# Kernel optimization log

Hardware: AMD Instinct MI355X
Metric: run time of the kernel (lower is better)

The kernel has to match this reference:

```python
import jax, jax.numpy as jnp
import numpy as np

B, N, C, NUM_HEADS = 4, 2048, 768, 12
HID = 4 * C
EPS = 1e-5


def _ln(x, g, b):
    m = x.mean(-1, keepdims=True)
    v = ((x - m) ** 2).mean(-1, keepdims=True)
    return (x - m) / jnp.sqrt(v + EPS) * g + b


def _attend(q, k, v, scale):
    # q,k,v: (B, H, N, D)
    scores = jnp.einsum('bhnd,bhmd->bhnm', q, k) * scale
    a = jax.nn.softmax(scores, axis=-1)
    return jnp.einsum('bhnm,bhmd->bhnd', a, v)


def _split_heads(t):
    b, n, c = t.shape
    return t.reshape(b, n, NUM_HEADS, c // NUM_HEADS).transpose(0, 2, 1, 3)


def _merge_heads(t):
    b, h, n, d = t.shape
    return t.transpose(0, 2, 1, 3).reshape(b, n, h * d)


def setup_inputs() -> dict:
    key = jax.random.key(0)
    ks = jax.random.split(key, 16)
    s = 0.02
    inp = {
        'x': jax.random.normal(ks[0], (B, N, C), jnp.float32),
        'y': jax.random.normal(ks[1], (B, N, C), jnp.float32),
        'xpos': jax.random.randint(ks[2], (B, N, 2), 0, 64, jnp.int32),
        'ypos': jax.random.randint(ks[3], (B, N, 2), 0, 64, jnp.int32),
        'g1': jnp.ones((C,)), 'be1': jnp.zeros((C,)),
        'g2': jnp.ones((C,)), 'be2': jnp.zeros((C,)),
        'g3': jnp.ones((C,)), 'be3': jnp.zeros((C,)),
        'gy': jnp.ones((C,)), 'bey': jnp.zeros((C,)),
        'Wqkv': jax.random.normal(ks[4], (C, 3 * C), jnp.float32) * s,
        'Wo_sa': jax.random.normal(ks[5], (C, C), jnp.float32) * s,
        'bo_sa': jnp.zeros((C,)),
        'Wq': jax.random.normal(ks[6], (C, C), jnp.float32) * s,
        'Wk': jax.random.normal(ks[7], (C, C), jnp.float32) * s,
        'Wv': jax.random.normal(ks[8], (C, C), jnp.float32) * s,
        'Wo_ca': jax.random.normal(ks[9], (C, C), jnp.float32) * s,
        'bo_ca': jnp.zeros((C,)),
        'W1': jax.random.normal(ks[10], (C, HID), jnp.float32) * s,
        'b1': jnp.zeros((HID,)),
        'W2': jax.random.normal(ks[11], (HID, C), jnp.float32) * s,
        'b2': jnp.zeros((C,)),
        'h': 32, 'w': 64,
    }
    return inp


def reference(x, y, xpos, ypos, g1, be1, g2, be2, g3, be3, gy, bey,
              Wqkv, Wo_sa, bo_sa, Wq, Wk, Wv, Wo_ca, bo_ca,
              W1, b1, W2, b2, h, w):
    scale = (C // NUM_HEADS) ** -0.5
    # --- self attention (rope=None, dropout=0, drop_path=0) ---
    xn = _ln(x, g1, be1)
    qkv = (xn @ Wqkv).reshape(x.shape[0], x.shape[1], 3, C)
    q, k, v = (_split_heads(qkv[:, :, i]) for i in range(3))
    o = _merge_heads(_attend(q, k, v, scale)) @ Wo_sa + bo_sa
    x = x + o
    # --- cross attention ---
    yn = _ln(y, gy, bey)
    xn2 = _ln(x, g2, be2)
    qc = _split_heads(xn2 @ Wq)
    kc = _split_heads(yn @ Wk)
    vc = _split_heads(yn @ Wv)
    oc = _merge_heads(_attend(qc, kc, vc, scale)) @ Wo_ca + bo_ca
    x = x + oc
    # --- MLP (exact GELU as torch nn.GELU default) ---
    xn3 = _ln(x, g3, be3)
    x = x + (jax.nn.gelu(xn3 @ W1 + b1, approximate=False) @ W2 + b2)
    return x
```

## Files before the change

### kernel.cpp

```cpp
#include <hip/hip_runtime.h>
#include <math.h>

typedef unsigned short u16;
typedef __attribute__((ext_vector_type(4))) float f32x4;
typedef __attribute__((ext_vector_type(8))) __bf16 bf16x8;
typedef __attribute__((ext_vector_type(8))) short s16x8;

#define AS1 __attribute__((address_space(1)))
#define AS3 __attribute__((address_space(3)))

__device__ __forceinline__ u16 cvt(float f) {
  __bf16 h = (__bf16)f;
  return *(u16*)&h;
}

__device__ __forceinline__ unsigned cvtpk(float lo, float hi) {
  unsigned r;
  asm("v_cvt_pk_bf16_f32 %0, %1, %2" : "=v"(r) : "v"(lo), "v"(hi));
  return r;
}

__device__ __forceinline__ float fexp2(float x) {
  float r;
  asm volatile("v_exp_f32 %0, %1" : "=v"(r) : "v"(x));
  return r;
}

__device__ __forceinline__ void load_lds16(const void* g, void* l) {
  __builtin_amdgcn_global_load_lds((AS1 void*)g, (AS3 void*)l, 16, 0, 0);
}

__device__ __forceinline__ f32x4 mfma16(bf16x8 a, bf16x8 b, f32x4 c) {
  return __builtin_amdgcn_mfma_f32_16x16x32_bf16(a, b, c, 0, 0, 0);
}

struct WT8 {
  const float* src[8];
  u16* dst[8];
  int K[8];
  int N[8];
  int cnt[8];
};

__global__ void wtrans_all(WT8 a) {
  __shared__ float t[32][33];
  int rem = blockIdx.x, i = 0;
  while (rem >= a.cnt[i]) { rem -= a.cnt[i]; ++i; }
  const int nb = a.N[i] >> 5;
  const int n0 = (rem % nb) * 32, k0 = (rem / nb) * 32;
  const float* W = a.src[i];
  u16* WT = a.dst[i];
  const int K = a.K[i], N = a.N[i];
  for (int r = threadIdx.y; r < 32; r += 8)
    t[r][threadIdx.x] = W[(size_t)(k0 + r) * N + n0 + threadIdx.x];
  __syncthreads();
  for (int r = threadIdx.y; r < 32; r += 8)
    WT[(size_t)(n0 + r) * K + k0 + threadIdx.x] = cvt(t[threadIdx.x][r]);
}

__global__ __launch_bounds__(256)
void ln_bf16(const float* __restrict__ in, const float* __restrict__ g,
             const float* __restrict__ be, u16* __restrict__ out) {
  const int row = blockIdx.x, tid = threadIdx.x;
  const float* x = in + (size_t)row * 768;
  float v0 = x[tid], v1 = x[tid + 256], v2 = x[tid + 512];
  float s = v0 + v1 + v2;
  for (int m = 1; m < 64; m <<= 1) s += __shfl_xor(s, m);
  __shared__ float red[8];
  const int w = tid >> 6, lane = tid & 63;
  if (lane == 0) red[w] = s;
  __syncthreads();
  s = red[0] + red[1] + red[2] + red[3];
  const float mean = s * (1.f / 768.f);
  const float d0 = v0 - mean, d1 = v1 - mean, d2 = v2 - mean;
  float q = d0 * d0 + d1 * d1 + d2 * d2;
  for (int m = 1; m < 64; m <<= 1) q += __shfl_xor(q, m);
  if (lane == 0) red[4 + w] = q;
  __syncthreads();
  q = red[4] + red[5] + red[6] + red[7];
  const float rstd = rsqrtf(q * (1.f / 768.f) + 1e-5f);
  u16* o = out + (size_t)row * 768;
  o[tid]       = cvt(d0 * rstd * g[tid]       + be[tid]);
  o[tid + 256] = cvt(d1 * rstd * g[tid + 256] + be[tid + 256]);
  o[tid + 512] = cvt(d2 * rstd * g[tid + 512] + be[tid + 512]);
}

template <int EPI, int BM>
__global__ __launch_bounds__(256, BM == 128 ? 2 : 3)
void gemm_bt(const u16* __restrict__ A, const u16* __restrict__ BT,
             const float* __restrict__ bias, const float* resid,
             void* outp, int M, int N, int K, int ldc) {
  constexpr int NI = (BM == 128) ? 4 : 2;
  constexpr int BK = (BM == 128) ? 32 : 64;
  __shared__ u16 As[BM * BK];
  __shared__ u16 Bs[128 * BK];
  const int tid = threadIdx.x;
  const int lane = tid & 63, w = tid >> 6;
  const int lr = lane & 15, g = lane >> 4;

  int bx = blockIdx.x, by = blockIdx.y;
  if (BM == 64) {
    const int nwg = gridDim.x * gridDim.y;
    if ((nwg & 7) == 0) {
      const int d = by * gridDim.x + bx;
      const int l = (d & 7) * (nwg >> 3) + (d >> 3);
      bx = l % gridDim.x;
      by = l / gridDim.x;
    }
  }
  const int row0 = by * BM, col0 = bx * 128;
  const int wm = (BM == 128) ? (w >> 1) * 64 : 0;
  const int wn = (BM == 128) ? (w & 1) * 64 : w * 32;

  f32x4 acc[4][NI] = {};

  if (BM == 128) {
    const int srow = lane >> 2, scol = (lane & 3) * 8;
    const int lk = g * 8;
    for (int k0 = 0; k0 < K; k0 += 32) {
#pragma unroll
      for (int i = 0; i < 2; ++i) {
        const int chunk = w * 2 + i;
        load_lds16(A + (size_t)(row0 + chunk * 16 + srow) * K + k0 + scol, &As[chunk * 512]);
        load_lds16(BT + (size_t)(col0 + chunk * 16 + srow) * K + k0 + scol, &Bs[chunk * 512]);
      }
      __syncthreads();
      bf16x8 af[4], bf[NI];
#pragma unroll
      for (int mi = 0; mi < 4; ++mi) af[mi] = *(const bf16x8*)&As[(wm + mi * 16 + lr) * 32 + lk];
#pragma unroll
      for (int ni = 0; ni < NI; ++ni) bf[ni] = *(const bf16x8*)&Bs[(wn + ni * 16 + lr) * 32 + lk];
#pragma unroll
      for (int mi = 0; mi < 4; ++mi)
#pragma unroll
        for (int ni = 0; ni < NI; ++ni)
          acc[mi][ni] = mfma16(af[mi], bf[ni], acc[mi][ni]);
      __syncthreads();
    }
  } else {
    for (int k0 = 0; k0 < K; k0 += 64) {
#pragma unroll
      for (int i = 0; i < 2; ++i) {
        const int ch = i * 256 + tid;
        const int r = ch >> 3, c = ch & 7, cs = c ^ (r & 7);
        load_lds16(A + (size_t)(row0 + r) * K + k0 + cs * 8, &As[ch * 8]);
      }
#pragma unroll
      for (int i = 0; i < 4; ++i) {
        const int ch = i * 256 + tid;
        const int r = ch >> 3, c = ch & 7, cs = c ^ (r & 7);
        load_lds16(BT + (size_t)(col0 + r) * K + k0 + cs * 8, &Bs[ch * 8]);
      }
      __syncthreads();
#pragma unroll
      for (int kk = 0; kk < 2; ++kk) {
        bf16x8 af[4], bf[NI];
#pragma unroll
        for (int mi = 0; mi < 4; ++mi) {
          const int r = mi * 16 + lr;
          af[mi] = *(const bf16x8*)&As[r * 64 + (((kk * 4 + g) ^ (r & 7)) * 8)];
        }
#pragma unroll
        for (int ni = 0; ni < NI; ++ni) {
          const int r = wn + ni * 16 + lr;
          bf[ni] = *(const bf16x8*)&Bs[r * 64 + (((kk * 4 + g) ^ (r & 7)) * 8)];
        }
#pragma unroll
        for (int mi = 0; mi < 4; ++mi)
#pragma unroll
          for (int ni = 0; ni < NI; ++ni)
            acc[mi][ni] = mfma16(af[mi], bf[ni], acc[mi][ni]);
      }
      __syncthreads();
    }
  }

  const int rbase = g * 4;
#pragma unroll
  for (int mi = 0; mi < 4; ++mi) {
#pragma unroll
    for (int ni = 0; ni < NI; ++ni) {
#pragma unroll
      for (int rr = 0; rr < 4; ++rr) {
        const int r = row0 + wm + mi * 16 + rbase + rr;
        const int c = col0 + wn + ni * 16 + lr;
        float v = acc[mi][ni][rr];
        if (EPI == 0) {
          ((u16*)outp)[(size_t)r * ldc + c] = cvt(v);
        } else if (EPI == 1) {
          ((float*)outp)[(size_t)r * ldc + c] = v + bias[c] + resid[(size_t)r * ldc + c];
        } else {
          v += bias[c];
          v = 0.5f * v * (1.f + erff(v * 0.70710678118654752f));
          ((u16*)outp)[(size_t)r * ldc + c] = cvt(v);
        }
      }
    }
  }
}

__global__ __launch_bounds__(256, 3)
void flash_attn(const u16* __restrict__ qk, const u16* __restrict__ vt, u16* __restrict__ out) {
  __shared__ u16 Ks[2][64 * 64];
  __shared__ u16 Vs[2][64 * 64];
  __shared__ u16 P[128 * 72];
  const int tid = threadIdx.x, lane = tid & 63, w = tid >> 6;
  const int b = blockIdx.z, h = blockIdx.y, qb = blockIdx.x;
  const u16* qp = qk + (size_t)b * 2048 * 1536 + h * 64;
  const u16* kp = qp + 768;
  const u16* vtp = vt + (size_t)(h * 64) * 8192 + b * 2048;
  const int lr = lane & 15, g = lane >> 4, lk = g * 8;
  const int qrow = qb * 128 + w * 32;

  bf16x8 qf[2][2];
#pragma unroll
  for (int gq = 0; gq < 2; ++gq) {
#pragma unroll
    for (int t = 0; t < 2; ++t) {
      s16x8 qr = *(const s16x8*)&qp[(size_t)(qrow + gq * 16 + lr) * 1536 + t * 32 + lk];
      bf16x8 f;
#pragma unroll
      for (int j = 0; j < 8; ++j) {
        unsigned u = (unsigned)(u16)qr[j] << 16;
        f[j] = (__bf16)(__uint_as_float(u) * 0.18033688f);
      }
      qf[gq][t] = f;
    }
  }

  bf16x8 onesf;
#pragma unroll
  for (int j = 0; j < 8; ++j) onesf[j] = (__bf16)1.0f;

  f32x4 o[2][4] = {};
  f32x4 o4[2] = {};
  float rowm[2] = {-1e30f, -1e30f};

#define STAGE(bi, kv)                                                          \
  do {                                                                         \
    _Pragma("unroll") for (int i_ = 0; i_ < 2; ++i_) {                         \
      const int ch = i_ * 256 + tid;                                           \
      const int r_ = ch >> 3, c_ = ch & 7, cs_ = c_ ^ (r_ & 7);                \
      load_lds16(kp + (size_t)((kv) + r_) * 1536 + cs_ * 8, &Ks[bi][ch * 8]);  \
      load_lds16(vtp + (size_t)r_ * 8192 + (kv) + cs_ * 8, &Vs[bi][ch * 8]);   \
    }                                                                          \
  } while (0)

  STAGE(0, 0);
  __syncthreads();
  int cur = 0;

  for (int kv0 = 0; kv0 < 2048; kv0 += 64) {
    if (kv0 + 64 < 2048) STAGE(cur ^ 1, kv0 + 64);

    f32x4 s[2][4] = {};
#pragma unroll
    for (int t = 0; t < 2; ++t) {
#pragma unroll
      for (int ni = 0; ni < 4; ++ni) {
        const int r = ni * 16 + lr;
        bf16x8 kf = *(const bf16x8*)&Ks[cur][r * 64 + ((4 * t + g) ^ (lr & 7)) * 8];
        s[0][ni] = mfma16(kf, qf[0][t], s[0][ni]);
        s[1][ni] = mfma16(kf, qf[1][t], s[1][ni]);
      }
    }

    float lm[2];
#pragma unroll
    for (int gq = 0; gq < 2; ++gq) {
      float m0 = fmaxf(fmaxf(s[gq][0][0], s[gq][0][1]), fmaxf(s[gq][0][2], s[gq][0][3]));
      float m1 = fmaxf(fmaxf(s[gq][1][0], s[gq][1][1]), fmaxf(s[gq][1][2], s[gq][1][3]));
      float m2 = fmaxf(fmaxf(s[gq][2][0], s[gq][2][1]), fmaxf(s[gq][2][2], s[gq][2][3]));
      float m3 = fmaxf(fmaxf(s[gq][3][0], s[gq][3][1]), fmaxf(s[gq][3][2], s[gq][3][3]));
      lm[gq] = fmaxf(fmaxf(m0, m1), fmaxf(m2, m3));
    }
    const int ok = (lm[0] <= rowm[0] + 8.f) & (lm[1] <= rowm[1] + 8.f);
    if (!__all(ok)) {
#pragma unroll
      for (int gq = 0; gq < 2; ++gq) {
        float v = lm[gq];
        v = fmaxf(v, __shfl_xor(v, 16));
        v = fmaxf(v, __shfl_xor(v, 32));
        const float mn = fmaxf(rowm[gq], v);
        const float alpha = fexp2(rowm[gq] - mn);
        rowm[gq] = mn;
#pragma unroll
        for (int di = 0; di < 4; ++di) o[gq][di] *= alpha;
        o4[gq] *= alpha;
      }
    }

    unsigned* Pw = (unsigned*)P;
#pragma unroll
    for (int gq = 0; gq < 2; ++gq) {
      const int qrl = w * 32 + gq * 16 + lr;
#pragma unroll
      for (int ni = 0; ni < 4; ++ni) {
#pragma unroll
        for (int r = 0; r < 2; ++r) {
          const float p0 = fexp2(s[gq][ni][2 * r] - rowm[gq]);
          const float p1 = fexp2(s[gq][ni][2 * r + 1] - rowm[gq]);
          Pw[(qrl * 72 + ni * 16 + 4 * g + 2 * r) >> 1] = cvtpk(p0, p1);
        }
      }
    }

#pragma unroll
    for (int t = 0; t < 2; ++t) {
      bf16x8 pb0 = *(const bf16x8*)&P[(w * 32 + lr) * 72 + t * 32 + g * 8];
      bf16x8 pb1 = *(const bf16x8*)&P[(w * 32 + 16 + lr) * 72 + t * 32 + g * 8];
#pragma unroll
      for (int di = 0; di < 4; ++di) {
        bf16x8 va = *(const bf16x8*)&Vs[cur][(di * 16 + lr) * 64 + ((4 * t + g) ^ (lr & 7)) * 8];
        o[0][di] = mfma16(va, pb0, o[0][di]);
        o[1][di] = mfma16(va, pb1, o[1][di]);
      }
      o4[0] = mfma16(onesf, pb0, o4[0]);
      o4[1] = mfma16(onesf, pb1, o4[1]);
    }

    __syncthreads();
    cur ^= 1;
  }
#undef STAGE

#pragma unroll
  for (int gq = 0; gq < 2; ++gq) {
    const float inv = 1.0f / o4[gq][0];
    const size_t n = (size_t)b * 2048 + qrow + gq * 16 + lr;
#pragma unroll
    for (int di = 0; di < 4; ++di) {
      uint2 uv;
      uv.x = cvtpk(o[gq][di][0] * inv, o[gq][di][1] * inv);
      uv.y = cvtpk(o[gq][di][2] * inv, o[gq][di][3] * inv);
      *(uint2*)&out[n * 768 + h * 64 + di * 16 + 4 * g] = uv;
    }
  }
}

extern "C" void kernel_launch(void* const* d_in, const int* in_sizes, int n_in,
                              void* d_out, int out_size, void* d_ws, size_t ws_size,
                              hipStream_t stream) {
  const float* x     = (const float*)d_in[0];
  const float* y     = (const float*)d_in[1];
  const float* g1    = (const float*)d_in[4];
  const float* be1   = (const float*)d_in[5];
  const float* g2    = (const float*)d_in[6];
  const float* be2   = (const float*)d_in[7];
  const float* g3    = (const float*)d_in[8];
  const float* be3   = (const float*)d_in[9];
  const float* gy    = (const float*)d_in[10];
  const float* bey   = (const float*)d_in[11];
  const float* Wqkv  = (const float*)d_in[12];
  const float* Wo_sa = (const float*)d_in[13];
  const float* bo_sa = (const float*)d_in[14];
  const float* Wq    = (const float*)d_in[15];
  const float* Wk    = (const float*)d_in[16];
  const float* Wv    = (const float*)d_in[17];
  const float* Wo_ca = (const float*)d_in[18];
  const float* bo_ca = (const float*)d_in[19];
  const float* W1    = (const float*)d_in[20];
  const float* b1    = (const float*)d_in[21];
  const float* W2    = (const float*)d_in[22];
  const float* b2    = (const float*)d_in[23];

  u16* WqkvT = (u16*)d_ws;
  u16* WoSaT = WqkvT + (size_t)2304 * 768;
  u16* WqT   = WoSaT + (size_t)768 * 768;
  u16* WkT   = WqT   + (size_t)768 * 768;
  u16* WvT   = WkT   + (size_t)768 * 768;
  u16* WoCaT = WvT   + (size_t)768 * 768;
  u16* W1T   = WoCaT + (size_t)768 * 768;
  u16* W2T   = W1T   + (size_t)3072 * 768;
  u16* R1    = W2T   + (size_t)768 * 3072;
  u16* VT    = R1    + (size_t)8192 * 1536;
  u16* R2    = R1    + (size_t)8192 * 3072;
  u16* R3    = R2    + (size_t)8192 * 768;
  float* xo  = (float*)d_out;

  WT8 wa;
  {
    const float* s8[8] = {Wqkv, Wo_sa, Wq, Wk, Wv, Wo_ca, W1, W2};
    u16* d8[8] = {WqkvT, WoSaT, WqT, WkT, WvT, WoCaT, W1T, W2T};
    const int K8[8] = {768, 768, 768, 768, 768, 768, 768, 3072};
    const int N8[8] = {2304, 768, 768, 768, 768, 768, 3072, 768};
    for (int i = 0; i < 8; ++i) {
      wa.src[i] = s8[i]; wa.dst[i] = d8[i];
      wa.K[i] = K8[i]; wa.N[i] = N8[i];
      wa.cnt[i] = (N8[i] / 32) * (K8[i] / 32);
    }
  }
  wtrans_all<<<9216, dim3(32, 8), 0, stream>>>(wa);

  ln_bf16<<<8192, 256, 0, stream>>>(x, g1, be1, R2);
  gemm_bt<0, 128><<<dim3(12, 64), 256, 0, stream>>>(R2, WqkvT, nullptr, nullptr, R1, 8192, 1536, 768, 1536);
  gemm_bt<0, 64><<<dim3(64, 12), 256, 0, stream>>>(WqkvT + (size_t)1536 * 768, R2, nullptr, nullptr, VT, 768, 8192, 768, 8192);
  flash_attn<<<dim3(16, 12, 4), 256, 0, stream>>>(R1, VT, R2);
  gemm_bt<1, 64><<<dim3(6, 128), 256, 0, stream>>>(R2, WoSaT, bo_sa, x, xo, 8192, 768, 768, 768);

  ln_bf16<<<8192, 256, 0, stream>>>(y, gy, bey, R3);
  ln_bf16<<<8192, 256, 0, stream>>>(xo, g2, be2, R2);
  gemm_bt<0, 64><<<dim3(6, 128), 256, 0, stream>>>(R2, WqT, nullptr, nullptr, R1, 8192, 768, 768, 1536);
  gemm_bt<0, 64><<<dim3(6, 128), 256, 0, stream>>>(R3, WkT, nullptr, nullptr, R1 + 768, 8192, 768, 768, 1536);
  gemm_bt<0, 64><<<dim3(64, 12), 256, 0, stream>>>(WvT, R3, nullptr, nullptr, VT, 768, 8192, 768, 8192);
  flash_attn<<<dim3(16, 12, 4), 256, 0, stream>>>(R1, VT, R3);
  gemm_bt<1, 64><<<dim3(6, 128), 256, 0, stream>>>(R3, WoCaT, bo_ca, xo, xo, 8192, 768, 768, 768);

  ln_bf16<<<8192, 256, 0, stream>>>(xo, g3, be3, R2);
  gemm_bt<2, 128><<<dim3(24, 64), 256, 0, stream>>>(R2, W1T, b1, nullptr, R1, 8192, 3072, 768, 3072);
  gemm_bt<1, 64><<<dim3(6, 128), 256, 0, stream>>>(R1, W2T, b2, xo, xo, 8192, 768, 3072, 768);
}
```

Before: 467.9 us.

## Unify GEMM on BK=64 swizzled path and tweak attention softmax stores

The BM=128 GEMM variant now uses the BK=64 XOR-swizzled LDS path instead of BK=32 unswizzled tiles, with launch bounds raised to 3 and the grid remapping applied to all tile sizes. In the attention kernel, P values are written as one 64-bit store per fragment instead of two 32-bit stores, and the max reduction is reshaped. The PV MFMA section is also wrapped in s_setprio to favor matrix issue. The larger LDS tile and higher occupancy target may raise register pressure for the 128-row GEMM.

```diff
diff --git a/kernel.cpp b/kernel.cpp
--- a/kernel.cpp
+++ b/kernel.cpp
@@ -86,20 +86,19 @@
 }
 
 template <int EPI, int BM>
-__global__ __launch_bounds__(256, BM == 128 ? 2 : 3)
+__global__ __launch_bounds__(256, 3)
 void gemm_bt(const u16* __restrict__ A, const u16* __restrict__ BT,
              const float* __restrict__ bias, const float* resid,
              void* outp, int M, int N, int K, int ldc) {
   constexpr int NI = (BM == 128) ? 4 : 2;
-  constexpr int BK = (BM == 128) ? 32 : 64;
-  __shared__ u16 As[BM * BK];
-  __shared__ u16 Bs[128 * BK];
+  __shared__ u16 As[BM * 64];
+  __shared__ u16 Bs[128 * 64];
   const int tid = threadIdx.x;
   const int lane = tid & 63, w = tid >> 6;
   const int lr = lane & 15, g = lane >> 4;
 
   int bx = blockIdx.x, by = blockIdx.y;
-  if (BM == 64) {
+  {
     const int nwg = gridDim.x * gridDim.y;
     if ((nwg & 7) == 0) {
       const int d = by * gridDim.x + bx;
@@ -114,65 +113,40 @@
 
   f32x4 acc[4][NI] = {};
 
-  if (BM == 128) {
-    const int srow = lane >> 2, scol = (lane & 3) * 8;
-    const int lk = g * 8;
-    for (int k0 = 0; k0 < K; k0 += 32) {
-#pragma unroll
-      for (int i = 0; i < 2; ++i) {
-        const int chunk = w * 2 + i;
-        load_lds16(A + (size_t)(row0 + chunk * 16 + srow) * K + k0 + scol, &As[chunk * 512]);
-        load_lds16(BT + (size_t)(col0 + chunk * 16 + srow) * K + k0 + scol, &Bs[chunk * 512]);
-      }
-      __syncthreads();
+  for (int k0 = 0; k0 < K; k0 += 64) {
+#pragma unroll
+    for (int i = 0; i < BM / 32; ++i) {
+      const int ch = i * 256 + tid;
+      const int r = ch >> 3, c = ch & 7, cs = c ^ (r & 7);
+      load_lds16(A + (size_t)(row0 + r) * K + k0 + cs * 8, &As[ch * 8]);
+    }
+#pragma unroll
+    for (int i = 0; i < 4; ++i) {
+      const int ch = i * 256 + tid;
+      const int r = ch >> 3, c = ch & 7, cs = c ^ (r & 7);
+      load_lds16(BT + (size_t)(col0 + r) * K + k0 + cs * 8, &Bs[ch * 8]);
+    }
+    __syncthreads();
+#pragma unroll
+    for (int kk = 0; kk < 2; ++kk) {
       bf16x8 af[4], bf[NI];
 #pragma unroll
-      for (int mi = 0; mi < 4; ++mi) af[mi] = *(const bf16x8*)&As[(wm + mi * 16 + lr) * 32 + lk];
-#pragma unroll
-      for (int ni = 0; ni < NI; ++ni) bf[ni] = *(const bf16x8*)&Bs[(wn + ni * 16 + lr) * 32 + lk];
+      for (int mi = 0; mi < 4; ++mi) {
+        const int r = wm + mi * 16 + lr;
+        af[mi] = *(const bf16x8*)&As[r * 64 + (((kk * 4 + g) ^ (lr & 7)) * 8)];
+      }
+#pragma unroll
+      for (int ni = 0; ni < NI; ++ni) {
+        const int r = wn + ni * 16 + lr;
+        bf[ni] = *(const bf16x8*)&Bs[r * 64 + (((kk * 4 + g) ^ (lr & 7)) * 8)];
+      }
 #pragma unroll
       for (int mi = 0; mi < 4; ++mi)
 #pragma unroll
         for (int ni = 0; ni < NI; ++ni)
           acc[mi][ni] = mfma16(af[mi], bf[ni], acc[mi][ni]);
-      __syncthreads();
-    }
-  } else {
-    for (int k0 = 0; k0 < K; k0 += 64) {
-#pragma unroll
-      for (int i = 0; i < 2; ++i) {
-        const int ch = i * 256 + tid;
-        const int r = ch >> 3, c = ch & 7, cs = c ^ (r & 7);
-        load_lds16(A + (size_t)(row0 + r) * K + k0 + cs * 8, &As[ch * 8]);
-      }
-#pragma unroll
-      for (int i = 0; i < 4; ++i) {
-        const int ch = i * 256 + tid;
-        const int r = ch >> 3, c = ch & 7, cs = c ^ (r & 7);
-        load_lds16(BT + (size_t)(col0 + r) * K + k0 + cs * 8, &Bs[ch * 8]);
-      }
-      __syncthreads();
-#pragma unroll
-      for (int kk = 0; kk < 2; ++kk) {
-        bf16x8 af[4], bf[NI];
-#pragma unroll
-        for (int mi = 0; mi < 4; ++mi) {
-          const int r = mi * 16 + lr;
-          af[mi] = *(const bf16x8*)&As[r * 64 + (((kk * 4 + g) ^ (r & 7)) * 8)];
-        }
-#pragma unroll
-        for (int ni = 0; ni < NI; ++ni) {
-          const int r = wn + ni * 16 + lr;
-          bf[ni] = *(const bf16x8*)&Bs[r * 64 + (((kk * 4 + g) ^ (r & 7)) * 8)];
-        }
-#pragma unroll
-        for (int mi = 0; mi < 4; ++mi)
-#pragma unroll
-          for (int ni = 0; ni < NI; ++ni)
-            acc[mi][ni] = mfma16(af[mi], bf[ni], acc[mi][ni]);
-      }
-      __syncthreads();
-    }
+    }
+    __syncthreads();
   }
 
   const int rbase = g * 4;
@@ -268,11 +242,12 @@
     float lm[2];
 #pragma unroll
     for (int gq = 0; gq < 2; ++gq) {
-      float m0 = fmaxf(fmaxf(s[gq][0][0], s[gq][0][1]), fmaxf(s[gq][0][2], s[gq][0][3]));
-      float m1 = fmaxf(fmaxf(s[gq][1][0], s[gq][1][1]), fmaxf(s[gq][1][2], s[gq][1][3]));
-      float m2 = fmaxf(fmaxf(s[gq][2][0], s[gq][2][1]), fmaxf(s[gq][2][2], s[gq][2][3]));
-      float m3 = fmaxf(fmaxf(s[gq][3][0], s[gq][3][1]), fmaxf(s[gq][3][2], s[gq][3][3]));
-      lm[gq] = fmaxf(fmaxf(m0, m1), fmaxf(m2, m3));
+      float a = fmaxf(fmaxf(s[gq][0][0], s[gq][0][1]), s[gq][0][2]);
+      float b2 = fmaxf(fmaxf(s[gq][0][3], s[gq][1][0]), s[gq][1][1]);
+      float c = fmaxf(fmaxf(s[gq][1][2], s[gq][1][3]), s[gq][2][0]);
+      float d = fmaxf(fmaxf(s[gq][2][1], s[gq][2][2]), s[gq][2][3]);
+      float e = fmaxf(fmaxf(s[gq][3][0], s[gq][3][1]), s[gq][3][2]);
+      lm[gq] = fmaxf(fmaxf(fmaxf(a, b2), fmaxf(c, d)), fmaxf(e, s[gq][3][3]));
     }
     const int ok = (lm[0] <= rowm[0] + 8.f) & (lm[1] <= rowm[1] + 8.f);
     if (!__all(ok)) {
@@ -290,21 +265,19 @@
       }
     }
 
-    unsigned* Pw = (unsigned*)P;
 #pragma unroll
     for (int gq = 0; gq < 2; ++gq) {
       const int qrl = w * 32 + gq * 16 + lr;
 #pragma unroll
       for (int ni = 0; ni < 4; ++ni) {
-#pragma unroll
-        for (int r = 0; r < 2; ++r) {
-          const float p0 = fexp2(s[gq][ni][2 * r] - rowm[gq]);
-          const float p1 = fexp2(s[gq][ni][2 * r + 1] - rowm[gq]);
-          Pw[(qrl * 72 + ni * 16 + 4 * g + 2 * r) >> 1] = cvtpk(p0, p1);
-        }
-      }
-    }
-
+        uint2 pv;
+        pv.x = cvtpk(fexp2(s[gq][ni][0] - rowm[gq]), fexp2(s[gq][ni][1] - rowm[gq]));
+        pv.y = cvtpk(fexp2(s[gq][ni][2] - rowm[gq]), fexp2(s[gq][ni][3] - rowm[gq]));
+        *(uint2*)&P[qrl * 72 + ni * 16 + 4 * g] = pv;
+      }
+    }
+
+    __builtin_amdgcn_s_setprio(1);
 #pragma unroll
     for (int t = 0; t < 2; ++t) {
       bf16x8 pb0 = *(const bf16x8*)&P[(w * 32 + lr) * 72 + t * 32 + g * 8];
@@ -318,6 +291,7 @@
       o4[0] = mfma16(onesf, pb0, o4[0]);
       o4[1] = mfma16(onesf, pb1, o4[1]);
     }
+    __builtin_amdgcn_s_setprio(0);
 
     __syncthreads();
     cur ^= 1;
```

New measurement: 461.0 us. About the same (-1.5%).
